# Performance work log

Measured on AMD Instinct MI355X. Metric: run time of the kernel, lower is better.

The kernel has to match this reference:

```python
import jax, jax.numpy as jnp
import numpy as np

N_NODES = 100000
N_EDGES = 1600000
IN_CH = 64
HID = 64
N_CLASSES = 10
N_GRAPHS = 64


def setup_inputs() -> dict:
    key = jax.random.key(0)
    ks = jax.random.split(key, 12)
    x = jax.random.normal(ks[0], (N_NODES, IN_CH), dtype=jnp.float32)
    edge_index = jax.random.randint(ks[1], (2, N_EDGES), 0, N_NODES, dtype=jnp.int64)
    batch = jnp.sort(jax.random.randint(ks[2], (N_NODES,), 0, N_GRAPHS, dtype=jnp.int64))
    def glorot(k, shape):
        lim = 1.0 / np.sqrt(shape[1])
        return jax.random.uniform(k, shape, dtype=jnp.float32, minval=-lim, maxval=lim)
    # GraphConv layer 1: lin_rel (with bias) and lin_root (no bias)
    W1_rel = glorot(ks[3], (HID, IN_CH))
    W1_root = glorot(ks[4], (HID, IN_CH))
    b1 = glorot(ks[5], (1, IN_CH))[0, :HID] * 0 + glorot(ks[5], (HID, 1))[:, 0]
    # GraphConv layer 2
    W2_rel = glorot(ks[6], (HID, HID))
    W2_root = glorot(ks[7], (HID, HID))
    b2 = glorot(ks[8], (HID, 1))[:, 0]
    # final classifier Linear
    W_lin = glorot(ks[9], (N_CLASSES, HID))
    b_lin = glorot(ks[10], (N_CLASSES, 1))[:, 0]
    return {
        "x": x, "edge_index": edge_index, "batch": batch,
        "W1_rel": W1_rel, "W1_root": W1_root, "b1": b1,
        "W2_rel": W2_rel, "W2_root": W2_root, "b2": b2,
        "W_lin": W_lin, "b_lin": b_lin,
    }


def _graph_conv(x, src, dst, W_rel, W_root, b):
    # PyG GraphConv: out_i = W_rel @ (sum_{j->i} x_j) + b + W_root @ x_i
    agg = jax.ops.segment_sum(x[src], dst, num_segments=N_NODES)  # [N, C]
    return agg @ W_rel.T + x @ W_root.T + b


def reference(x, edge_index, batch, W1_rel, W1_root, b1, W2_rel, W2_root, b2, W_lin, b_lin):
    src, dst = edge_index[0], edge_index[1]
    h = jax.nn.relu(_graph_conv(x, src, dst, W1_rel, W1_root, b1))
    h = jax.nn.relu(_graph_conv(h, src, dst, W2_rel, W2_root, b2))
    # global mean pool over graph ids
    sums = jax.ops.segment_sum(h, batch, num_segments=N_GRAPHS)          # [G, H]
    counts = jax.ops.segment_sum(jnp.ones((h.shape[0],), h.dtype), batch, num_segments=N_GRAPHS)
    pooled = sums / jnp.maximum(counts, 1.0)[:, None]
    return pooled @ W_lin.T + b_lin  # [G, num_classes]
```

## Files before the change

kernel.cpp:

```cpp
#include <hip/hip_runtime.h>

typedef unsigned short u16;
typedef __attribute__((ext_vector_type(8))) short bf16x8;
typedef __attribute__((ext_vector_type(4))) float f32x4;

constexpr int CH = 64;
constexpr int NG = 64;
constexpr int NC = 10;
constexpr int SHIFT = 9;
constexpr int BW = 1 << SHIFT;
constexpr int EPW = 8192;

__device__ __forceinline__ void f4add(float4& a, const float4 v) {
    a.x += v.x; a.y += v.y; a.z += v.z; a.w += v.w;
}
__device__ __forceinline__ u16 f2bf(float f) {
    unsigned u = __float_as_uint(f);
    u = (u + 0x7FFFu + ((u >> 16) & 1u)) >> 16;
    return (u16)u;
}
__device__ __forceinline__ void bfacc(float4& a, unsigned lo, unsigned hi) {
    a.x += __uint_as_float(lo << 16);
    a.y += __uint_as_float(lo & 0xFFFF0000u);
    a.z += __uint_as_float(hi << 16);
    a.w += __uint_as_float(hi & 0xFFFF0000u);
}

__global__ __launch_bounds__(256) void k_bucket(const int* __restrict__ src,
                                                const int* __restrict__ dst,
                                                int* __restrict__ bcnt,
                                                int* __restrict__ bbuf,
                                                int nb, int cap, int n_edges)
{
    __shared__ int hist[256];
    __shared__ int cur[256];
    int t = threadIdx.x;
    int e0 = blockIdx.x * EPW;
    int e1 = min(e0 + EPW, n_edges);
    if (t < nb) hist[t] = 0;
    __syncthreads();
    for (int e = e0 + t; e < e1; e += 256)
        atomicAdd(&hist[dst[e] >> SHIFT], 1);
    __syncthreads();
    if (t < nb) cur[t] = atomicAdd(&bcnt[t], hist[t]);
    __syncthreads();
    for (int e = e0 + t; e < e1; e += 256) {
        int d = dst[e];
        int b = d >> SHIFT;
        int pos = atomicAdd(&cur[b], 1);
        if (pos < cap)
            bbuf[(size_t)b * cap + pos] = src[e] | ((d & (BW - 1)) << 17);
    }
}

__global__ __launch_bounds__(256) void k_build(const int* __restrict__ bbuf,
                                               const int* __restrict__ bcnt,
                                               int* __restrict__ rowptr,
                                               int* __restrict__ csr,
                                               int nb, int cap, int n)
{
    __shared__ int sc[256];
    __shared__ int hist[BW];
    __shared__ int cur[BW];
    __shared__ int psum[256];
    int b = blockIdx.x;
    int t = threadIdx.x;
    int v = (t < nb) ? min(bcnt[t], cap) : 0;
    sc[t] = v;
    __syncthreads();
    for (int off = 1; off < 256; off <<= 1) {
        int u = (t >= off) ? sc[t - off] : 0;
        __syncthreads();
        sc[t] += u;
        __syncthreads();
    }
    if (b == 0 && t == nb - 1) rowptr[n] = sc[t];
    int cnt = min(bcnt[b], cap);
    int base = sc[b] - cnt;
    __syncthreads();
    const int* mybuf = bbuf + (size_t)b * cap;
    hist[t] = 0; hist[t + 256] = 0;
    __syncthreads();
    for (int i = t; i < cnt; i += 256)
        atomicAdd(&hist[mybuf[i] >> 17], 1);
    __syncthreads();
    int h0 = hist[2 * t], h1 = hist[2 * t + 1];
    int ps = h0 + h1;
    psum[t] = ps;
    __syncthreads();
    for (int off = 1; off < 256; off <<= 1) {
        int u = (t >= off) ? psum[t - off] : 0;
        __syncthreads();
        psum[t] += u;
        __syncthreads();
    }
    int e0 = psum[t] - ps;
    int nodeBase = b * BW;
    cur[2 * t]     = base + e0;
    cur[2 * t + 1] = base + e0 + h0;
    if (nodeBase + 2 * t < n)     rowptr[nodeBase + 2 * t]     = base + e0;
    if (nodeBase + 2 * t + 1 < n) rowptr[nodeBase + 2 * t + 1] = base + e0 + h0;
    __syncthreads();
    for (int i = t; i < cnt; i += 256) {
        int vv = mybuf[i];
        int pos = atomicAdd(&cur[vv >> 17], 1);
        csr[pos] = vv & 0x1FFFF;
    }
}

template<bool BF16IN>
__global__ __launch_bounds__(256) void k_xform_mfma(const void* in_,
                                                    const float* __restrict__ Wrel,
                                                    const float* __restrict__ Wroot,
                                                    const float* __restrict__ bias,
                                                    u16* __restrict__ Y,
                                                    u16* R, int n, int ngroups)
{
    if (blockIdx.x == 0 && threadIdx.x < 64)
        Y[(size_t)n * CH + threadIdx.x] = 0;

    int lane = threadIdx.x & 63;
    int lr = lane & 15;
    int g  = lane >> 4;

    bf16x8 wf[2][4][2];
    const float* Wm[2] = { Wrel, Wroot };
#pragma unroll
    for (int m = 0; m < 2; ++m)
#pragma unroll
        for (int t = 0; t < 4; ++t)
#pragma unroll
            for (int kt = 0; kt < 2; ++kt) {
                const float* p = Wm[m] + (16 * t + lr) * CH + 32 * kt + 8 * g;
                bf16x8 v;
#pragma unroll
                for (int j = 0; j < 8; ++j) v[j] = (short)f2bf(p[j]);
                wf[m][t][kt] = v;
            }
    float bvt[4];
#pragma unroll
    for (int t = 0; t < 4; ++t) bvt[t] = bias[16 * t + lr];

    int wid = blockIdx.x * 4 + (threadIdx.x >> 6);
#pragma unroll
    for (int gi = 0; gi < 2; ++gi) {
        int grp = wid * 2 + gi;
        if (grp >= ngroups) return;
        int gbase = grp * 16;
        int arow = gbase + lr;
        if (arow >= n) arow = n - 1;

        bf16x8 af[2];
#pragma unroll
        for (int kt = 0; kt < 2; ++kt) {
            if (BF16IN) {
                const u16* hp = (const u16*)in_ + (size_t)arow * CH + kt * 32 + 8 * g;
                af[kt] = *(const bf16x8*)hp;
            } else {
                const float* xp = (const float*)in_ + (size_t)arow * CH + kt * 32 + 8 * g;
                bf16x8 v;
#pragma unroll
                for (int j = 0; j < 8; ++j) v[j] = (short)f2bf(xp[j]);
                af[kt] = v;
            }
        }

        f32x4 z = { 0.f, 0.f, 0.f, 0.f };
        f32x4 aY[4] = { z, z, z, z };
        f32x4 aR[4] = { z, z, z, z };
#pragma unroll
        for (int kt = 0; kt < 2; ++kt)
#pragma unroll
            for (int t = 0; t < 4; ++t) {
                aY[t] = __builtin_amdgcn_mfma_f32_16x16x32_bf16(af[kt], wf[0][t][kt], aY[t], 0, 0, 0);
                aR[t] = __builtin_amdgcn_mfma_f32_16x16x32_bf16(af[kt], wf[1][t][kt], aR[t], 0, 0, 0);
            }

#pragma unroll
        for (int t = 0; t < 4; ++t)
#pragma unroll
            for (int r = 0; r < 4; ++r) {
                int node = gbase + 4 * g + r;
                if (node < n) {
                    Y[(size_t)node * CH + 16 * t + lr] = f2bf(aY[t][r]);
                    R[(size_t)node * CH + 16 * t + lr] = f2bf(aR[t][r] + bvt[t]);
                }
            }
    }
}

template<bool POOL>
__global__ __launch_bounds__(256) void k_gather5(const u16* __restrict__ Y,
                                                 const int* __restrict__ rowptr,
                                                 const int* __restrict__ csr,
                                                 u16* RO,
                                                 const int* __restrict__ batch,
                                                 float* __restrict__ sums,
                                                 int n, int chunk)
{
    int lane = threadIdx.x & 63;
    int grp = lane >> 4, sub = lane & 15;
    int wid = blockIdx.x * 4 + (threadIdx.x >> 6);
    int nb = wid * chunk, ne = min(nb + chunk, n);
    if (nb >= n) return;
    float4 run = make_float4(0, 0, 0, 0);
    int gcur = -1;
    int e0 = rowptr[nb];
    for (int node = nb; node < ne; ++node) {
        int e1 = rowptr[node + 1];
        uint2 pr = *(const uint2*)(RO + (size_t)node * CH + sub * 4);
        float4 a0 = make_float4(0, 0, 0, 0), a1 = a0;
        int e = e0;
        for (; e + 16 <= e1; e += 16) {
            int s0 = csr[e + grp],      s1 = csr[e + 4 + grp];
            int s2 = csr[e + 8 + grp],  s3 = csr[e + 12 + grp];
            uint2 p0 = *(const uint2*)(Y + (size_t)s0 * CH + sub * 4);
            uint2 p1 = *(const uint2*)(Y + (size_t)s1 * CH + sub * 4);
            uint2 p2 = *(const uint2*)(Y + (size_t)s2 * CH + sub * 4);
            uint2 p3 = *(const uint2*)(Y + (size_t)s3 * CH + sub * 4);
            bfacc(a0, p0.x, p0.y); bfacc(a1, p1.x, p1.y);
            bfacc(a0, p2.x, p2.y); bfacc(a1, p3.x, p3.y);
        }
        if (e < e1) {
            int s0 = (e + grp      < e1) ? csr[e + grp]      : n;
            int s1 = (e + 4 + grp  < e1) ? csr[e + 4 + grp]  : n;
            int s2 = (e + 8 + grp  < e1) ? csr[e + 8 + grp]  : n;
            int s3 = (e + 12 + grp < e1) ? csr[e + 12 + grp] : n;
            uint2 p0 = *(const uint2*)(Y + (size_t)s0 * CH + sub * 4);
            uint2 p1 = *(const uint2*)(Y + (size_t)s1 * CH + sub * 4);
            uint2 p2 = *(const uint2*)(Y + (size_t)s2 * CH + sub * 4);
            uint2 p3 = *(const uint2*)(Y + (size_t)s3 * CH + sub * 4);
            bfacc(a0, p0.x, p0.y); bfacc(a1, p1.x, p1.y);
            bfacc(a0, p2.x, p2.y); bfacc(a1, p3.x, p3.y);
        }
        e0 = e1;
        f4add(a0, a1);
        a0.x += __shfl_xor(a0.x, 16); a0.y += __shfl_xor(a0.y, 16);
        a0.z += __shfl_xor(a0.z, 16); a0.w += __shfl_xor(a0.w, 16);
        a0.x += __shfl_xor(a0.x, 32); a0.y += __shfl_xor(a0.y, 32);
        a0.z += __shfl_xor(a0.z, 32); a0.w += __shfl_xor(a0.w, 32);
        float4 r = make_float4(0, 0, 0, 0);
        bfacc(r, pr.x, pr.y);
        float4 h;
        h.x = fmaxf(a0.x + r.x, 0.f); h.y = fmaxf(a0.y + r.y, 0.f);
        h.z = fmaxf(a0.z + r.z, 0.f); h.w = fmaxf(a0.w + r.w, 0.f);
        if (!POOL) {
            if (grp == 0) {
                uint2 o;
                o.x = (unsigned)f2bf(h.x) | ((unsigned)f2bf(h.y) << 16);
                o.y = (unsigned)f2bf(h.z) | ((unsigned)f2bf(h.w) << 16);
                *(uint2*)(RO + (size_t)node * CH + sub * 4) = o;
            }
        } else {
            int g = batch[node];
            if (g != gcur) {
                if (gcur >= 0 && grp == 0) {
                    float* s = sums + gcur * CH + sub * 4;
                    atomicAdd(s + 0, run.x); atomicAdd(s + 1, run.y);
                    atomicAdd(s + 2, run.z); atomicAdd(s + 3, run.w);
                }
                run = make_float4(0, 0, 0, 0);
                gcur = g;
            }
            f4add(run, h);
        }
    }
    if (POOL && gcur >= 0 && grp == 0) {
        float* s = sums + gcur * CH + sub * 4;
        atomicAdd(s + 0, run.x); atomicAdd(s + 1, run.y);
        atomicAdd(s + 2, run.z); atomicAdd(s + 3, run.w);
    }
}

__global__ void k_final(const float* __restrict__ sums,
                        const int* __restrict__ batch,
                        const float* __restrict__ Wlin,
                        const float* __restrict__ blin,
                        float* __restrict__ out, int n_nodes)
{
    int t = threadIdx.x;
    if (t >= NG * NC) return;
    int g = t / NC, c = t % NC;
    int lo = 0, hi = n_nodes;
    while (lo < hi) { int mid = (lo + hi) >> 1; if (batch[mid] < g) lo = mid + 1; else hi = mid; }
    int lb = lo;
    lo = 0; hi = n_nodes;
    while (lo < hi) { int mid = (lo + hi) >> 1; if (batch[mid] < g + 1) lo = mid + 1; else hi = mid; }
    int cnt = lo - lb;
    float inv = 1.0f / fmaxf((float)cnt, 1.0f);
    float acc = blin[c];
    for (int k = 0; k < CH; ++k)
        acc += sums[g * CH + k] * inv * Wlin[c * CH + k];
    out[g * NC + c] = acc;
}

extern "C" void kernel_launch(void* const* d_in, const int* in_sizes, int n_in,
                              void* d_out, int out_size, void* d_ws, size_t ws_size,
                              hipStream_t stream)
{
    const float* x      = (const float*)d_in[0];
    const int*   ei     = (const int*)d_in[1];
    const int*   batch  = (const int*)d_in[2];
    const float* W1rel  = (const float*)d_in[3];
    const float* W1root = (const float*)d_in[4];
    const float* b1     = (const float*)d_in[5];
    const float* W2rel  = (const float*)d_in[6];
    const float* W2root = (const float*)d_in[7];
    const float* b2     = (const float*)d_in[8];
    const float* Wlin   = (const float*)d_in[9];
    const float* blin   = (const float*)d_in[10];
    float* out = (float*)d_out;

    int n_nodes = in_sizes[0] / CH;
    int n_edges = in_sizes[1] / 2;
    const int* src = ei;
    const int* dst = ei + n_edges;

    int nb  = (n_nodes + BW - 1) >> SHIFT;
    int cap = n_edges / nb + 2048;

    u16*   Ybf    = (u16*)d_ws;
    u16*   Rbf    = Ybf + (size_t)(n_nodes + 1) * CH;
    int*   rowptr = (int*)(Rbf + (size_t)n_nodes * CH);
    int*   csr    = rowptr + (n_nodes + 1);
    int*   bbuf   = csr + n_edges + 16;
    int*   bcnt   = bbuf + (size_t)nb * cap;
    float* sums   = (float*)(bcnt + 256);

    hipMemsetAsync(bcnt, 0, 256 * sizeof(int), stream);
    int b1blocks = (n_edges + EPW - 1) / EPW;
    k_bucket<<<b1blocks, 256, 0, stream>>>(src, dst, bcnt, bbuf, nb, cap, n_edges);
    k_build<<<nb, 256, 0, stream>>>(bbuf, bcnt, rowptr, csr, nb, cap, n_nodes);

    int ngroups16 = (n_nodes + 15) / 16;
    int xblocks = (ngroups16 + 7) / 8;

    int waves = 2048 * 4;
    int chunk = (n_nodes + waves - 1) / waves;

    k_xform_mfma<false><<<xblocks, 256, 0, stream>>>(x, W1rel, W1root, b1,
                                                     Ybf, Rbf, n_nodes, ngroups16);
    k_gather5<false><<<2048, 256, 0, stream>>>(Ybf, rowptr, csr, Rbf,
                                               batch, sums, n_nodes, chunk);

    k_xform_mfma<true><<<xblocks, 256, 0, stream>>>(Rbf, W2rel, W2root, b2,
                                                    Ybf, Rbf, n_nodes, ngroups16);
    hipMemsetAsync(sums, 0, NG * CH * sizeof(float), stream);
    k_gather5<true><<<2048, 256, 0, stream>>>(Ybf, rowptr, csr, Rbf,
                                              batch, sums, n_nodes, chunk);

    k_final<<<1, NG * NC, 0, stream>>>(sums, batch, Wlin, blin, out, n_nodes);
}
```

Before: 228.3 us.

## Fuse edge bucketing with layer-1 transform; parallelize final classifier across blocks

The edge-bucketing kernel and the first layer's MFMA feature transform are merged into one launch, with disjoint block ranges, so the two independent stages overlap and one launch is removed. The final pooling/linear kernel now uses one 64-thread block per graph, computing dot products with wavefront shuffle reductions instead of serial per-thread loops. The fused kernel's shared-memory footprint and register use become the union of both bodies, which may lower occupancy for the bucketing part.

```diff
diff --git a/kernel.cpp b/kernel.cpp
--- a/kernel.cpp
+++ b/kernel.cpp
@@ -26,16 +26,17 @@
     a.w += __uint_as_float(hi & 0xFFFF0000u);
 }
 
-__global__ __launch_bounds__(256) void k_bucket(const int* __restrict__ src,
-                                                const int* __restrict__ dst,
-                                                int* __restrict__ bcnt,
-                                                int* __restrict__ bbuf,
-                                                int nb, int cap, int n_edges)
+__device__ __forceinline__ void bucket_body(int bid,
+                                            const int* __restrict__ src,
+                                            const int* __restrict__ dst,
+                                            int* __restrict__ bcnt,
+                                            int* __restrict__ bbuf,
+                                            int nb, int cap, int n_edges)
 {
     __shared__ int hist[256];
     __shared__ int cur[256];
     int t = threadIdx.x;
-    int e0 = blockIdx.x * EPW;
+    int e0 = bid * EPW;
     int e1 = min(e0 + EPW, n_edges);
     if (t < nb) hist[t] = 0;
     __syncthreads();
@@ -51,6 +52,115 @@
         if (pos < cap)
             bbuf[(size_t)b * cap + pos] = src[e] | ((d & (BW - 1)) << 17);
     }
+}
+
+template<bool BF16IN>
+__device__ __forceinline__ void xform_body(int bid, const void* in_,
+                                           const float* __restrict__ Wrel,
+                                           const float* __restrict__ Wroot,
+                                           const float* __restrict__ bias,
+                                           u16* __restrict__ Y,
+                                           u16* R, int n, int ngroups)
+{
+    if (bid == 0 && threadIdx.x < 64)
+        Y[(size_t)n * CH + threadIdx.x] = 0;
+
+    int lane = threadIdx.x & 63;
+    int lr = lane & 15;
+    int g  = lane >> 4;
+
+    bf16x8 wf[2][4][2];
+    const float* Wm[2] = { Wrel, Wroot };
+#pragma unroll
+    for (int m = 0; m < 2; ++m)
+#pragma unroll
+        for (int t = 0; t < 4; ++t)
+#pragma unroll
+            for (int kt = 0; kt < 2; ++kt) {
+                const float* p = Wm[m] + (16 * t + lr) * CH + 32 * kt + 8 * g;
+                bf16x8 v;
+#pragma unroll
+                for (int j = 0; j < 8; ++j) v[j] = (short)f2bf(p[j]);
+                wf[m][t][kt] = v;
+            }
+    float bvt[4];
+#pragma unroll
+    for (int t = 0; t < 4; ++t) bvt[t] = bias[16 * t + lr];
+
+    int wid = bid * 4 + (threadIdx.x >> 6);
+#pragma unroll
+    for (int gi = 0; gi < 2; ++gi) {
+        int grp = wid * 2 + gi;
+        if (grp >= ngroups) return;
+        int gbase = grp * 16;
+        int arow = gbase + lr;
+        if (arow >= n) arow = n - 1;
+
+        bf16x8 af[2];
+#pragma unroll
+        for (int kt = 0; kt < 2; ++kt) {
+            if (BF16IN) {
+                const u16* hp = (const u16*)in_ + (size_t)arow * CH + kt * 32 + 8 * g;
+                af[kt] = *(const bf16x8*)hp;
+            } else {
+                const float* xp = (const float*)in_ + (size_t)arow * CH + kt * 32 + 8 * g;
+                bf16x8 v;
+#pragma unroll
+                for (int j = 0; j < 8; ++j) v[j] = (short)f2bf(xp[j]);
+                af[kt] = v;
+            }
+        }
+
+        f32x4 z = { 0.f, 0.f, 0.f, 0.f };
+        f32x4 aY[4] = { z, z, z, z };
+        f32x4 aR[4] = { z, z, z, z };
+#pragma unroll
+        for (int kt = 0; kt < 2; ++kt)
+#pragma unroll
+            for (int t = 0; t < 4; ++t) {
+                aY[t] = __builtin_amdgcn_mfma_f32_16x16x32_bf16(af[kt], wf[0][t][kt], aY[t], 0, 0, 0);
+                aR[t] = __builtin_amdgcn_mfma_f32_16x16x32_bf16(af[kt], wf[1][t][kt], aR[t], 0, 0, 0);
+            }
+
+#pragma unroll
+        for (int t = 0; t < 4; ++t)
+#pragma unroll
+            for (int r = 0; r < 4; ++r) {
+                int node = gbase + 4 * g + r;
+                if (node < n) {
+                    Y[(size_t)node * CH + 16 * t + lr] = f2bf(aY[t][r]);
+                    R[(size_t)node * CH + 16 * t + lr] = f2bf(aR[t][r] + bvt[t]);
+                }
+            }
+    }
+}
+
+__global__ __launch_bounds__(256) void k_bx(const int* __restrict__ src,
+                                            const int* __restrict__ dst,
+                                            int* __restrict__ bcnt,
+                                            int* __restrict__ bbuf,
+                                            int nb, int cap, int n_edges,
+                                            const float* __restrict__ x,
+                                            const float* __restrict__ Wrel,
+                                            const float* __restrict__ Wroot,
+                                            const float* __restrict__ bias,
+                                            u16* __restrict__ Y,
+                                            u16* R, int n, int ngroups, int xoff)
+{
+    if ((int)blockIdx.x < xoff)
+        bucket_body(blockIdx.x, src, dst, bcnt, bbuf, nb, cap, n_edges);
+    else
+        xform_body<false>(blockIdx.x - xoff, x, Wrel, Wroot, bias, Y, R, n, ngroups);
+}
+
+__global__ __launch_bounds__(256) void k_xform2(const u16* in_,
+                                                const float* __restrict__ Wrel,
+                                                const float* __restrict__ Wroot,
+                                                const float* __restrict__ bias,
+                                                u16* __restrict__ Y,
+                                                u16* R, int n, int ngroups)
+{
+    xform_body<true>(blockIdx.x, in_, Wrel, Wroot, bias, Y, R, n, ngroups);
 }
 
 __global__ __launch_bounds__(256) void k_build(const int* __restrict__ bbuf,
@@ -105,87 +215,6 @@
         int vv = mybuf[i];
         int pos = atomicAdd(&cur[vv >> 17], 1);
         csr[pos] = vv & 0x1FFFF;
-    }
-}
-
-template<bool BF16IN>
-__global__ __launch_bounds__(256) void k_xform_mfma(const void* in_,
-                                                    const float* __restrict__ Wrel,
-                                                    const float* __restrict__ Wroot,
-                                                    const float* __restrict__ bias,
-                                                    u16* __restrict__ Y,
-                                                    u16* R, int n, int ngroups)
-{
-    if (blockIdx.x == 0 && threadIdx.x < 64)
-        Y[(size_t)n * CH + threadIdx.x] = 0;
-
-    int lane = threadIdx.x & 63;
-    int lr = lane & 15;
-    int g  = lane >> 4;
-
-    bf16x8 wf[2][4][2];
-    const float* Wm[2] = { Wrel, Wroot };
-#pragma unroll
-    for (int m = 0; m < 2; ++m)
-#pragma unroll
-        for (int t = 0; t < 4; ++t)
-#pragma unroll
-            for (int kt = 0; kt < 2; ++kt) {
-                const float* p = Wm[m] + (16 * t + lr) * CH + 32 * kt + 8 * g;
-                bf16x8 v;
-#pragma unroll
-                for (int j = 0; j < 8; ++j) v[j] = (short)f2bf(p[j]);
-                wf[m][t][kt] = v;
-            }
-    float bvt[4];
-#pragma unroll
-    for (int t = 0; t < 4; ++t) bvt[t] = bias[16 * t + lr];
-
-    int wid = blockIdx.x * 4 + (threadIdx.x >> 6);
-#pragma unroll
-    for (int gi = 0; gi < 2; ++gi) {
-        int grp = wid * 2 + gi;
-        if (grp >= ngroups) return;
-        int gbase = grp * 16;
-        int arow = gbase + lr;
-        if (arow >= n) arow = n - 1;
-
-        bf16x8 af[2];
-#pragma unroll
-        for (int kt = 0; kt < 2; ++kt) {
-            if (BF16IN) {
-                const u16* hp = (const u16*)in_ + (size_t)arow * CH + kt * 32 + 8 * g;
-                af[kt] = *(const bf16x8*)hp;
-            } else {
-                const float* xp = (const float*)in_ + (size_t)arow * CH + kt * 32 + 8 * g;
-                bf16x8 v;
-#pragma unroll
-                for (int j = 0; j < 8; ++j) v[j] = (short)f2bf(xp[j]);
-                af[kt] = v;
-            }
-        }
-
-        f32x4 z = { 0.f, 0.f, 0.f, 0.f };
-        f32x4 aY[4] = { z, z, z, z };
-        f32x4 aR[4] = { z, z, z, z };
-#pragma unroll
-        for (int kt = 0; kt < 2; ++kt)
-#pragma unroll
-            for (int t = 0; t < 4; ++t) {
-                aY[t] = __builtin_amdgcn_mfma_f32_16x16x32_bf16(af[kt], wf[0][t][kt], aY[t], 0, 0, 0);
-                aR[t] = __builtin_amdgcn_mfma_f32_16x16x32_bf16(af[kt], wf[1][t][kt], aR[t], 0, 0, 0);
-            }
-
-#pragma unroll
-        for (int t = 0; t < 4; ++t)
-#pragma unroll
-            for (int r = 0; r < 4; ++r) {
-                int node = gbase + 4 * g + r;
-                if (node < n) {
-                    Y[(size_t)node * CH + 16 * t + lr] = f2bf(aY[t][r]);
-                    R[(size_t)node * CH + 16 * t + lr] = f2bf(aR[t][r] + bvt[t]);
-                }
-            }
     }
 }
 
@@ -272,15 +301,14 @@
     }
 }
 
-__global__ void k_final(const float* __restrict__ sums,
-                        const int* __restrict__ batch,
-                        const float* __restrict__ Wlin,
-                        const float* __restrict__ blin,
-                        float* __restrict__ out, int n_nodes)
-{
-    int t = threadIdx.x;
-    if (t >= NG * NC) return;
-    int g = t / NC, c = t % NC;
+__global__ __launch_bounds__(64) void k_final2(const float* __restrict__ sums,
+                                               const int* __restrict__ batch,
+                                               const float* __restrict__ Wlin,
+                                               const float* __restrict__ blin,
+                                               float* __restrict__ out, int n_nodes)
+{
+    int g = blockIdx.x;
+    int l = threadIdx.x;
     int lo = 0, hi = n_nodes;
     while (lo < hi) { int mid = (lo + hi) >> 1; if (batch[mid] < g) lo = mid + 1; else hi = mid; }
     int lb = lo;
@@ -288,10 +316,14 @@
     while (lo < hi) { int mid = (lo + hi) >> 1; if (batch[mid] < g + 1) lo = mid + 1; else hi = mid; }
     int cnt = lo - lb;
     float inv = 1.0f / fmaxf((float)cnt, 1.0f);
-    float acc = blin[c];
-    for (int k = 0; k < CH; ++k)
-        acc += sums[g * CH + k] * inv * Wlin[c * CH + k];
-    out[g * NC + c] = acc;
+    float v = sums[g * CH + l] * inv;
+#pragma unroll
+    for (int c = 0; c < NC; ++c) {
+        float p = v * Wlin[c * CH + l];
+        p += __shfl_xor(p, 1);  p += __shfl_xor(p, 2);  p += __shfl_xor(p, 4);
+        p += __shfl_xor(p, 8);  p += __shfl_xor(p, 16); p += __shfl_xor(p, 32);
+        if (l == 0) out[g * NC + c] = p + blin[c];
+    }
 }
 
 extern "C" void kernel_launch(void* const* d_in, const int* in_sizes, int n_in,
@@ -323,31 +355,31 @@
     u16*   Rbf    = Ybf + (size_t)(n_nodes + 1) * CH;
     int*   rowptr = (int*)(Rbf + (size_t)n_nodes * CH);
     int*   csr    = rowptr + (n_nodes + 1);
-    int*   bbuf   = csr + n_edges + 16;
+    int*   bbuf   = csr + n_edges + 32;
     int*   bcnt   = bbuf + (size_t)nb * cap;
     float* sums   = (float*)(bcnt + 256);
 
-    hipMemsetAsync(bcnt, 0, 256 * sizeof(int), stream);
-    int b1blocks = (n_edges + EPW - 1) / EPW;
-    k_bucket<<<b1blocks, 256, 0, stream>>>(src, dst, bcnt, bbuf, nb, cap, n_edges);
-    k_build<<<nb, 256, 0, stream>>>(bbuf, bcnt, rowptr, csr, nb, cap, n_nodes);
-
     int ngroups16 = (n_nodes + 15) / 16;
     int xblocks = (ngroups16 + 7) / 8;
+    int b1blocks = (n_edges + EPW - 1) / EPW;
 
     int waves = 2048 * 4;
     int chunk = (n_nodes + waves - 1) / waves;
 
-    k_xform_mfma<false><<<xblocks, 256, 0, stream>>>(x, W1rel, W1root, b1,
-                                                     Ybf, Rbf, n_nodes, ngroups16);
+    hipMemsetAsync(bcnt, 0, 256 * sizeof(int), stream);
+    k_bx<<<b1blocks + xblocks, 256, 0, stream>>>(src, dst, bcnt, bbuf, nb, cap, n_edges,
+                                                 x, W1rel, W1root, b1,
+                                                 Ybf, Rbf, n_nodes, ngroups16, b1blocks);
+    k_build<<<nb, 256, 0, stream>>>(bbuf, bcnt, rowptr, csr, nb, cap, n_nodes);
+
     k_gather5<false><<<2048, 256, 0, stream>>>(Ybf, rowptr, csr, Rbf,
                                                batch, sums, n_nodes, chunk);
 
-    k_xform_mfma<true><<<xblocks, 256, 0, stream>>>(Rbf, W2rel, W2root, b2,
-                                                    Ybf, Rbf, n_nodes, ngroups16);
+    k_xform2<<<xblocks, 256, 0, stream>>>(Rbf, W2rel, W2root, b2,
+                                          Ybf, Rbf, n_nodes, ngroups16);
     hipMemsetAsync(sums, 0, NG * CH * sizeof(float), stream);
     k_gather5<true><<<2048, 256, 0, stream>>>(Ybf, rowptr, csr, Rbf,
                                               batch, sums, n_nodes, chunk);
 
-    k_final<<<1, NG * NC, 0, stream>>>(sums, batch, Wlin, blin, out, n_nodes);
-}
+    k_final2<<<NG, 64, 0, stream>>>(sums, batch, Wlin, blin, out, n_nodes);
+}
```

Measured after the change: 212.3 us. -7.0%, faster.
